# Kernel optimization log

Hardware: AMD Instinct MI355X
Metric: run time of the kernel (lower is better)

Reference implementation:

```python
import jax, jax.numpy as jnp
import numpy as np


def setup_inputs() -> dict:
    key = jax.random.key(0)
    k1, k2, k3 = jax.random.split(key, 3)
    N, D, H, E = 8192, 1024, 1024, 16
    scale = 1.0 / np.sqrt(D)
    return {
        "x": jax.random.normal(k1, (N, D), dtype=jnp.float32),
        "router_w": jax.random.normal(k2, (D, E), dtype=jnp.float32) * scale,
        "router_b": jnp.zeros((E,), dtype=jnp.float32),
        "expert_w": jax.random.normal(k3, (E, D, H), dtype=jnp.float32) * scale,
        "expert_b": jnp.zeros((E, H), dtype=jnp.float32),
        "k": 2,
    }


def reference(x, router_w, router_b, expert_w, expert_b, k):
    # Router: softmax over experts, then top-k.
    logits = x @ router_w + router_b                      # [N, E]
    routing_weights = jax.nn.softmax(logits, axis=-1)     # [N, E]
    top_k_weights, top_k_indices = jax.lax.top_k(routing_weights, k)  # [N, k]

    # Dense all-expert compute (faithful to original): [N, E, H]
    expert_outputs = jnp.einsum('nd,edh->neh', x, expert_w) + expert_b[None, :, :]

    # Gather top-k expert outputs: [N, k, H]
    gathered = jnp.take_along_axis(expert_outputs, top_k_indices[:, :, None], axis=1)

    # Weighted sum over k (weights NOT renormalized, as in the original).
    out = jnp.sum(top_k_weights[:, :, None] * gathered, axis=1)  # [N, H]
    return out
```

## Files before the change

### kernel.cpp

```cpp
#include <hip/hip_runtime.h>
#include <hip/hip_bf16.h>


#define N_TOK 8192
#define D_DIM 1024
#define H_DIM 1024
#define E_NUM 16
#define CAP   1024
#define KPAD  40

typedef __attribute__((ext_vector_type(4))) float f32x4;
typedef __attribute__((ext_vector_type(8))) short bf16x8;

__device__ __forceinline__ unsigned short f2bf(float f) {
    unsigned int u = __float_as_uint(f);
    unsigned int r = u + 0x7fffu + ((u >> 16) & 1u);
    return (unsigned short)(r >> 16);
}
__device__ __forceinline__ unsigned int pk2bf(float lo, float hi) {
    return (unsigned int)f2bf(lo) | ((unsigned int)f2bf(hi) << 16);
}

__global__ __launch_bounds__(256, 4) void router_kernel(
    const float* __restrict__ x,
    const float* __restrict__ rw,
    const float* __restrict__ rb,
    int4* __restrict__ res)
{
    const int wave = threadIdx.x >> 6;
    const int lane = threadIdx.x & 63;
    const int ds   = lane >> 4;
    const int e    = lane & 15;
    const int t0   = blockIdx.x * 8 + wave * 2;

    const float* x0  = x + (size_t)t0 * D_DIM + ds * 256;
    const float* x1  = x0 + D_DIM;
    const float* rwp = rw + ds * 4096 + e;

    double acc0 = 0.0, acc1 = 0.0;
#pragma unroll 2
    for (int g = 0; g < 8; ++g) {
        float s0 = 0.0f, s1 = 0.0f;
#pragma unroll
        for (int u = 0; u < 8; ++u) {
            const int jb = g * 8 + u;
            const float4 a = *(const float4*)(x0 + jb * 4);
            const float4 b = *(const float4*)(x1 + jb * 4);
            const float w0 = rwp[jb * 64];
            const float w1 = rwp[jb * 64 + 16];
            const float w2 = rwp[jb * 64 + 32];
            const float w3 = rwp[jb * 64 + 48];
            s0 = fmaf(a.w, w3, fmaf(a.z, w2, fmaf(a.y, w1, fmaf(a.x, w0, s0))));
            s1 = fmaf(b.w, w3, fmaf(b.z, w2, fmaf(b.y, w1, fmaf(b.x, w0, s1))));
        }
        acc0 += (double)s0;
        acc1 += (double)s1;
    }

    double v0 = acc0, v1 = acc1;
    v0 += __shfl_xor(v0, 16); v0 += __shfl_xor(v0, 32);
    v1 += __shfl_xor(v1, 16); v1 += __shfl_xor(v1, 32);

    __shared__ double lg[4][2][E_NUM];
    if (ds == 0) {
        const double bias = (double)rb[e];
        lg[wave][0][e] = v0 + bias;
        lg[wave][1][e] = v1 + bias;
    }
    __syncthreads();

    if (lane < 2) {
        const double* L = lg[wave][lane];
        double m = L[0];
#pragma unroll
        for (int k = 1; k < E_NUM; ++k) m = fmax(m, L[k]);

        int e1 = 0;
#pragma unroll
        for (int k = 1; k < E_NUM; ++k) if (L[k] > L[e1]) e1 = k;
        int e2 = (e1 == 0) ? 1 : 0;
        for (int k = 0; k < E_NUM; ++k)
            if (k != e1 && L[k] > L[e2]) e2 = k;

        float s = 0.0f;
#pragma unroll
        for (int k = 0; k < E_NUM; ++k) s = fmaf(expf((float)(L[k] - m)), 1.0f, s);
        const float w1 = expf((float)(L[e1] - m)) / s;
        const float w2 = expf((float)(L[e2] - m)) / s;

        const int n = t0 + lane;
        res[n] = make_int4(e1, e2, __float_as_int(w1), __float_as_int(w2));
    }
}

__global__ __launch_bounds__(256) void build_lists(
    const int4* __restrict__ res,
    int* __restrict__ counts0, int* __restrict__ counts1,
    int2* __restrict__ entries0, int2* __restrict__ entries1)
{
    const int e = blockIdx.x;
    __shared__ int c0, c1;
    if (threadIdx.x == 0) { c0 = 0; c1 = 0; }
    __syncthreads();

    for (int i = threadIdx.x; i < N_TOK; i += 256) {
        const int4 r = res[i];
        if (r.x == e) {
            int p = atomicAdd(&c0, 1);
            if (p < CAP) entries0[e * CAP + p] = make_int2(i, r.z);
        }
        if (r.y == e) {
            int p = atomicAdd(&c1, 1);
            if (p < CAP) entries1[e * CAP + p] = make_int2(i, r.w);
        }
    }
    __syncthreads();
    if (threadIdx.x == 0) { counts0[e] = c0; counts1[e] = c1; }
}

template <bool ADD>
__global__ __launch_bounds__(256) void moe_mfma_kernel(
    const float* __restrict__ x,
    const float* __restrict__ ew,
    const float* __restrict__ eb,
    const int* __restrict__ counts,
    const int2* __restrict__ entries,
    float* __restrict__ out)
{
    const int e = blockIdx.z;
    int count = counts[e];
    if (count > CAP) count = CAP;
    const int i0 = blockIdx.y * 128;
    if (i0 >= count) return;
    const int h0 = blockIdx.x * 128;

    __shared__ unsigned short Xs[128][KPAD];
    __shared__ unsigned short Ws[128][KPAD];
    __shared__ int   s_tok[128];
    __shared__ float s_w[128];

    const int tid = threadIdx.x;
    if (tid < 128) {
        const int i = i0 + tid;
        if (i < count) {
            int2 en = entries[e * CAP + i];
            s_tok[tid] = en.x;
            s_w[tid] = __int_as_float(en.y);
        } else {
            s_tok[tid] = 0;
            s_w[tid] = 0.0f;
        }
    }
    __syncthreads();

    const int wave = tid >> 6;
    const int lane = tid & 63;
    const int wr = (wave >> 1) * 64;
    const int wc = (wave & 1) * 64;
    const int l15 = lane & 15;
    const int quad = lane >> 4;

    f32x4 acc[4][4] = {};

    const int a_kq = (tid & 7) * 4;
    const int a_r0 = tid >> 3;
    const int b_n  = tid & 127;
    const int b_dh = (tid >> 7) * 16;

    const float* wcol = ew + (size_t)e * D_DIM * H_DIM + h0 + b_n;

    for (int d0 = 0; d0 < D_DIM; d0 += 32) {
#pragma unroll
        for (int it = 0; it < 4; ++it) {
            const int r = a_r0 + it * 32;
            const float4 v = *(const float4*)(x + (size_t)s_tok[r] * D_DIM + d0 + a_kq);
            ushort4 p;
            p.x = f2bf(v.x); p.y = f2bf(v.y); p.z = f2bf(v.z); p.w = f2bf(v.w);
            *(ushort4*)&Xs[r][a_kq] = p;
        }
        {
            float t[16];
#pragma unroll
            for (int i = 0; i < 16; ++i)
                t[i] = wcol[(size_t)(d0 + b_dh + i) * H_DIM];
            uint4 lo, hi;
            lo.x = pk2bf(t[0], t[1]);  lo.y = pk2bf(t[2], t[3]);
            lo.z = pk2bf(t[4], t[5]);  lo.w = pk2bf(t[6], t[7]);
            hi.x = pk2bf(t[8], t[9]);  hi.y = pk2bf(t[10], t[11]);
            hi.z = pk2bf(t[12], t[13]); hi.w = pk2bf(t[14], t[15]);
            *(uint4*)&Ws[b_n][b_dh]     = lo;
            *(uint4*)&Ws[b_n][b_dh + 8] = hi;
        }
        __syncthreads();

        bf16x8 af[4], bq[4];
#pragma unroll
        for (int i = 0; i < 4; ++i)
            af[i] = *(const bf16x8*)&Xs[wr + i * 16 + l15][quad * 8];
#pragma unroll
        for (int j = 0; j < 4; ++j)
            bq[j] = *(const bf16x8*)&Ws[wc + j * 16 + l15][quad * 8];
#pragma unroll
        for (int i = 0; i < 4; ++i)
#pragma unroll
            for (int j = 0; j < 4; ++j)
                acc[i][j] = __builtin_amdgcn_mfma_f32_16x16x32_bf16(
                    af[i], bq[j], acc[i][j], 0, 0, 0);

        __syncthreads();
    }

    float bias_j[4];
    const float* ebp = eb + e * H_DIM + h0 + wc;
#pragma unroll
    for (int j = 0; j < 4; ++j) bias_j[j] = ebp[j * 16 + l15];

#pragma unroll
    for (int i = 0; i < 4; ++i) {
#pragma unroll
        for (int r = 0; r < 4; ++r) {
            const int row = wr + i * 16 + quad * 4 + r;
            if (i0 + row < count) {
                const int tok = s_tok[row];
                const float w = s_w[row];
                float* op = out + (size_t)tok * H_DIM + h0 + wc + l15;
#pragma unroll
                for (int j = 0; j < 4; ++j) {
                    float v = w * (acc[i][j][r] + bias_j[j]);
                    if (ADD) v += op[j * 16];
                    op[j * 16] = v;
                }
            }
        }
    }
}

extern "C" void kernel_launch(void* const* d_in, const int* in_sizes, int n_in,
                              void* d_out, int out_size, void* d_ws, size_t ws_size,
                              hipStream_t stream)
{
    const float* x  = (const float*)d_in[0];
    const float* rw = (const float*)d_in[1];
    const float* rb = (const float*)d_in[2];
    const float* ew = (const float*)d_in[3];
    const float* eb = (const float*)d_in[4];

    char* ws = (char*)d_ws;
    int*  counts0  = (int*)ws;
    int*  counts1  = (int*)(ws + 64);
    int2* entries0 = (int2*)(ws + 1024);
    int2* entries1 = (int2*)(ws + 1024 + E_NUM * CAP * 8);

    int4* res = (int4*)d_out;

    router_kernel<<<N_TOK / 8, 256, 0, stream>>>(x, rw, rb, res);

    build_lists<<<E_NUM, 256, 0, stream>>>(res, counts0, counts1,
                                           entries0, entries1);

    dim3 grid(H_DIM / 128, CAP / 128, E_NUM);
    moe_mfma_kernel<false><<<grid, 256, 0, stream>>>(
        x, ew, eb, counts0, entries0, (float*)d_out);
    moe_mfma_kernel<true><<<grid, 256, 0, stream>>>(
        x, ew, eb, counts1, entries1, (float*)d_out);
}
```

Baseline: 332.9 us.

## Double-buffer LDS tiles with register prefetch and remap block order across XCDs

```diff
diff --git a/kernel.cpp b/kernel.cpp
--- a/kernel.cpp
+++ b/kernel.cpp
@@ -127,15 +127,18 @@
     const int2* __restrict__ entries,
     float* __restrict__ out)
 {
-    const int e = blockIdx.z;
+    const int flat = blockIdx.x;
+    const int lid  = (flat & 7) * 128 + (flat >> 3);
+    const int h0 = (lid & 7) * 128;
+    const int i0 = ((lid >> 3) & 7) * 128;
+    const int e  = lid >> 6;
+
     int count = counts[e];
     if (count > CAP) count = CAP;
-    const int i0 = blockIdx.y * 128;
     if (i0 >= count) return;
-    const int h0 = blockIdx.x * 128;
-
-    __shared__ unsigned short Xs[128][KPAD];
-    __shared__ unsigned short Ws[128][KPAD];
+
+    __shared__ unsigned short Xs[2][128][KPAD];
+    __shared__ unsigned short Ws[2][128][KPAD];
     __shared__ int   s_tok[128];
     __shared__ float s_w[128];
 
@@ -167,39 +170,58 @@
     const int b_n  = tid & 127;
     const int b_dh = (tid >> 7) * 16;
 
-    const float* wcol = ew + (size_t)e * D_DIM * H_DIM + h0 + b_n;
-
+    const float* ap[4];
+#pragma unroll
+    for (int it = 0; it < 4; ++it)
+        ap[it] = x + (size_t)s_tok[a_r0 + it * 32] * D_DIM + a_kq;
+    const float* bp = ew + (size_t)e * D_DIM * H_DIM
+                    + (size_t)b_dh * H_DIM + h0 + b_n;
+
+    float4 pa[4];
+    float  pb[16];
+#pragma unroll
+    for (int it = 0; it < 4; ++it) pa[it] = *(const float4*)(ap[it]);
+#pragma unroll
+    for (int i = 0; i < 16; ++i)  pb[i] = bp[(size_t)i * H_DIM];
+
+    {
+#pragma unroll
+        for (int it = 0; it < 4; ++it) {
+            ushort4 p;
+            p.x = f2bf(pa[it].x); p.y = f2bf(pa[it].y);
+            p.z = f2bf(pa[it].z); p.w = f2bf(pa[it].w);
+            *(ushort4*)&Xs[0][a_r0 + it * 32][a_kq] = p;
+        }
+        uint4 lo, hi;
+        lo.x = pk2bf(pb[0], pb[1]);   lo.y = pk2bf(pb[2], pb[3]);
+        lo.z = pk2bf(pb[4], pb[5]);   lo.w = pk2bf(pb[6], pb[7]);
+        hi.x = pk2bf(pb[8], pb[9]);   hi.y = pk2bf(pb[10], pb[11]);
+        hi.z = pk2bf(pb[12], pb[13]); hi.w = pk2bf(pb[14], pb[15]);
+        *(uint4*)&Ws[0][b_n][b_dh]     = lo;
+        *(uint4*)&Ws[0][b_n][b_dh + 8] = hi;
+    }
+
+    int cur = 0;
     for (int d0 = 0; d0 < D_DIM; d0 += 32) {
-#pragma unroll
-        for (int it = 0; it < 4; ++it) {
-            const int r = a_r0 + it * 32;
-            const float4 v = *(const float4*)(x + (size_t)s_tok[r] * D_DIM + d0 + a_kq);
-            ushort4 p;
-            p.x = f2bf(v.x); p.y = f2bf(v.y); p.z = f2bf(v.z); p.w = f2bf(v.w);
-            *(ushort4*)&Xs[r][a_kq] = p;
-        }
-        {
-            float t[16];
+        __syncthreads();
+        const bool more = (d0 + 32 < D_DIM);
+
+        if (more) {
+#pragma unroll
+            for (int it = 0; it < 4; ++it)
+                pa[it] = *(const float4*)(ap[it] + d0 + 32);
 #pragma unroll
             for (int i = 0; i < 16; ++i)
-                t[i] = wcol[(size_t)(d0 + b_dh + i) * H_DIM];
-            uint4 lo, hi;
-            lo.x = pk2bf(t[0], t[1]);  lo.y = pk2bf(t[2], t[3]);
-            lo.z = pk2bf(t[4], t[5]);  lo.w = pk2bf(t[6], t[7]);
-            hi.x = pk2bf(t[8], t[9]);  hi.y = pk2bf(t[10], t[11]);
-            hi.z = pk2bf(t[12], t[13]); hi.w = pk2bf(t[14], t[15]);
-            *(uint4*)&Ws[b_n][b_dh]     = lo;
-            *(uint4*)&Ws[b_n][b_dh + 8] = hi;
-        }
-        __syncthreads();
+                pb[i] = bp[(size_t)(d0 + 32 + i) * H_DIM];
+        }
 
         bf16x8 af[4], bq[4];
 #pragma unroll
         for (int i = 0; i < 4; ++i)
-            af[i] = *(const bf16x8*)&Xs[wr + i * 16 + l15][quad * 8];
+            af[i] = *(const bf16x8*)&Xs[cur][wr + i * 16 + l15][quad * 8];
 #pragma unroll
         for (int j = 0; j < 4; ++j)
-            bq[j] = *(const bf16x8*)&Ws[wc + j * 16 + l15][quad * 8];
+            bq[j] = *(const bf16x8*)&Ws[cur][wc + j * 16 + l15][quad * 8];
 #pragma unroll
         for (int i = 0; i < 4; ++i)
 #pragma unroll
@@ -207,7 +229,24 @@
                 acc[i][j] = __builtin_amdgcn_mfma_f32_16x16x32_bf16(
                     af[i], bq[j], acc[i][j], 0, 0, 0);
 
-        __syncthreads();
+        if (more) {
+            const int nxt = cur ^ 1;
+#pragma unroll
+            for (int it = 0; it < 4; ++it) {
+                ushort4 p;
+                p.x = f2bf(pa[it].x); p.y = f2bf(pa[it].y);
+                p.z = f2bf(pa[it].z); p.w = f2bf(pa[it].w);
+                *(ushort4*)&Xs[nxt][a_r0 + it * 32][a_kq] = p;
+            }
+            uint4 lo, hi;
+            lo.x = pk2bf(pb[0], pb[1]);   lo.y = pk2bf(pb[2], pb[3]);
+            lo.z = pk2bf(pb[4], pb[5]);   lo.w = pk2bf(pb[6], pb[7]);
+            hi.x = pk2bf(pb[8], pb[9]);   hi.y = pk2bf(pb[10], pb[11]);
+            hi.z = pk2bf(pb[12], pb[13]); hi.w = pk2bf(pb[14], pb[15]);
+            *(uint4*)&Ws[nxt][b_n][b_dh]     = lo;
+            *(uint4*)&Ws[nxt][b_n][b_dh + 8] = hi;
+        }
+        cur ^= 1;
     }
 
     float bias_j[4];
@@ -258,9 +297,8 @@
     build_lists<<<E_NUM, 256, 0, stream>>>(res, counts0, counts1,
                                            entries0, entries1);
 
-    dim3 grid(H_DIM / 128, CAP / 128, E_NUM);
-    moe_mfma_kernel<false><<<grid, 256, 0, stream>>>(
+    moe_mfma_kernel<false><<<1024, 256, 0, stream>>>(
         x, ew, eb, counts0, entries0, (float*)d_out);
-    moe_mfma_kernel<true><<<grid, 256, 0, stream>>>(
+    moe_mfma_kernel<true><<<1024, 256, 0, stream>>>(
         x, ew, eb, counts1, entries1, (float*)d_out);
 }
```

After: 330.4 us. No clear change (-0.8%).
